# Performance work log

Hardware: AMD Instinct MI355X
Metric: run time of the kernel (lower is better)

Reference implementation:

```python
import jax, jax.numpy as jnp
import numpy as np

V = 32000   # vocab.size
E = 512     # embed_dim
H = 512     # hidden_dim
L = 2       # num_layers
W = 32      # window_size
S = 512     # seq_len
B = 8       # batch


def setup_inputs() -> dict:
    key = jax.random.key(0)
    ks = jax.random.split(key, 2 + 4 * L)
    bound = 1.0 / np.sqrt(H)
    inp = {
        "encoder_input": jax.random.randint(ks[0], (S, B), 0, V),
        "embed_table": jax.random.normal(ks[1], (V, E), jnp.float32),
    }
    for l in range(L):
        in_dim = E if l == 0 else H
        k = ks[2 + 4 * l: 6 + 4 * l]
        inp[f"w_ih_{l}"] = jax.random.uniform(k[0], (4 * H, in_dim), jnp.float32, -bound, bound)
        inp[f"w_hh_{l}"] = jax.random.uniform(k[1], (4 * H, H), jnp.float32, -bound, bound)
        inp[f"b_ih_{l}"] = jax.random.uniform(k[2], (4 * H,), jnp.float32, -bound, bound)
        inp[f"b_hh_{l}"] = jax.random.uniform(k[3], (4 * H,), jnp.float32, -bound, bound)
    return inp


def _lstm_layer(x, mask, w_ih, w_hh, b_ih, b_hh):
    # x: [T, N, D]; mask: [T, N, 1]. Masked steps keep (h, c), so every window
    # effectively starts from a zero state at its first valid position (same as
    # running a fresh LSTM on each window, torch gate order i,f,g,o).
    N = x.shape[1]
    Hd = w_hh.shape[1]
    bias = b_ih + b_hh

    def step(carry, inp_):
        h, c = carry
        xt, mt = inp_
        gates = xt @ w_ih.T + h @ w_hh.T + bias  # [N, 4H]
        i, f, g, o = jnp.split(gates, 4, axis=-1)
        i = jax.nn.sigmoid(i)
        f = jax.nn.sigmoid(f)
        g = jnp.tanh(g)
        o = jax.nn.sigmoid(o)
        c_new = f * c + i * g
        h_new = o * jnp.tanh(c_new)
        h = jnp.where(mt, h_new, h)
        c = jnp.where(mt, c_new, c)
        return (h, c), h

    z = jnp.zeros((N, Hd), x.dtype)
    (h, _), ys = jax.lax.scan(step, (z, z), (x, mask))
    return ys, h


def reference(encoder_input, embed_table,
              w_ih_0, w_hh_0, b_ih_0, b_hh_0,
              w_ih_1, w_hh_1, b_ih_1, b_hh_1):
    emb = embed_table[encoder_input]              # [S, B, E]
    T = W + 1
    # window position t for target index i is i - W + t (invalid when < 0)
    pos = jnp.arange(S)[None, :] - W + jnp.arange(T)[:, None]  # [T, S]
    valid = pos >= 0
    windows = emb[jnp.clip(pos, 0)]               # [T, S, B, E]
    x = windows.reshape(T, S * B, E)
    mask = jnp.broadcast_to(valid[:, :, None], (T, S, B)).reshape(T, S * B, 1)

    params = [(w_ih_0, w_hh_0, b_ih_0, b_hh_0), (w_ih_1, w_hh_1, b_ih_1, b_hh_1)]
    h = None
    for (wi, wh, bi, bh) in params:
        x, h = _lstm_layer(x, mask, wi, wh, bi, bh)
    # original takes encoder_output at the last window position == final hidden
    return h.reshape(S, B, H)
```

## Files before the change

kernel.cpp:

```cpp
#include <hip/hip_runtime.h>
#include <stdint.h>

#define NROWS 4096
#define HDIM  512
#define GDIM  2048
#define WWIN  32

typedef __attribute__((ext_vector_type(8))) short short8;
typedef __attribute__((ext_vector_type(4))) float f32x4;

__device__ __forceinline__ unsigned short f2bf(float x){
  union { float f; unsigned int u; } v; v.f = x;
  unsigned int u = v.u + 0x7fffu + ((v.u >> 16) & 1u);
  return (unsigned short)(u >> 16);
}
__device__ __forceinline__ float bf2f(unsigned short u){
  union { unsigned int u; float f; } v; v.u = ((unsigned int)u) << 16; return v.f;
}

__device__ __forceinline__ void gld16(const void* g, void* l){
  __builtin_amdgcn_global_load_lds(
      (const __attribute__((address_space(1))) unsigned int*)g,
      (__attribute__((address_space(3))) unsigned int*)l, 16, 0, 0);
}

__device__ __forceinline__ float sigm(float x){ return 1.f/(1.f + __expf(-x)); }
__device__ __forceinline__ float tanh_f(float x){ return 1.f - 2.f/(1.f + __expf(2.f*x)); }

__device__ __forceinline__ void band_sync(unsigned* ctr, unsigned target){
  __syncthreads();
  if (threadIdx.x == 0){
    __hip_atomic_fetch_add(ctr, 1u, __ATOMIC_RELAXED, __HIP_MEMORY_SCOPE_AGENT);
    while (__hip_atomic_load(ctr, __ATOMIC_RELAXED, __HIP_MEMORY_SCOPE_AGENT) < target)
      __builtin_amdgcn_s_sleep(2);
  }
  asm volatile("" ::: "memory");
  __syncthreads();
}

__device__ __forceinline__ void gemm_tile_db(
    const char* A0, const char* A1, const char* Bsrc,
    int ldbB, int nk, int r0, int c0,
    char* smem, int wr, int wc, int lane, f32x4 acc[4][4])
{
  const int tid = threadIdx.x;
  const int oo0 = tid * 16;
  const int srow = oo0 >> 7;
  const int scb  = oo0 & 127;
  const size_t aOff = (size_t)(r0 + srow) * 1024 + scb;
  const size_t bOff = (size_t)(c0 + srow) * (size_t)ldbB + scb;

  auto STAGE = [&](int kk, int buf){
    const char* Ap = (kk < 8) ? A0 : A1;
    const size_t kbA = (size_t)(kk & 7) * 128;
    const size_t kbB = (size_t)kk * 128;
    char* AsB = smem + buf * 16384;
    char* BsB = smem + 32768 + buf * 16384;
    #pragma unroll
    for (int i = 0; i < 4; ++i){
      const size_t rstep = (size_t)i * 32;
      gld16(Ap   + aOff + rstep * 1024          + kbA, AsB + i*4096 + oo0);
      gld16(Bsrc + bOff + rstep * (size_t)ldbB  + kbB, BsB + i*4096 + oo0);
    }
  };

  STAGE(0, 0);
  __syncthreads();

  const int lr = lane & 15;
  const int lk = (lane >> 4) * 8;

  for (int kk = 0; kk < nk; ++kk){
    const int cur = kk & 1;
    if (kk + 1 < nk) STAGE(kk + 1, cur ^ 1);

    const unsigned short* As = (const unsigned short*)(smem + cur*16384);
    const unsigned short* Bs = (const unsigned short*)(smem + 32768 + cur*16384);
    short8 a[2][4], b[2][4];
    #pragma unroll
    for (int h = 0; h < 2; ++h){
      const int k32 = h * 32;
      #pragma unroll
      for (int m = 0; m < 4; ++m)
        a[h][m] = *(const short8*)(As + (64*wr + 16*m + lr)*64 + k32 + lk);
      #pragma unroll
      for (int n = 0; n < 4; ++n)
        b[h][n] = *(const short8*)(Bs + (64*wc + 16*n + lr)*64 + k32 + lk);
    }
    __builtin_amdgcn_s_setprio(1);
    #pragma unroll
    for (int h = 0; h < 2; ++h)
      #pragma unroll
      for (int m = 0; m < 4; ++m)
        #pragma unroll
        for (int n = 0; n < 4; ++n)
          acc[m][n] = __builtin_amdgcn_mfma_f32_16x16x32_bf16(a[h][m], b[h][n], acc[m][n], 0, 0, 0);
    __builtin_amdgcn_s_setprio(0);

    __syncthreads();
  }
}

__global__ void __launch_bounds__(256) prep_weights(
    const float* wih0, const float* whh0, const float* bih0, const float* bhh0,
    const float* wih1, const float* whh1, const float* bih1, const float* bhh1,
    unsigned short* BrIh0, unsigned short* Br0, unsigned short* Br1,
    float* bias0r, float* br1)
{
  const int j = blockIdx.x;
  const int g = j & 3, hd = j >> 2;
  const int r = g*512 + hd;
  for (int k = threadIdx.x; k < 512; k += 256){
    BrIh0[(size_t)j*512 + k]      = f2bf(wih0[(size_t)r*512 + k]);
    Br0  [(size_t)j*512 + k]      = f2bf(whh0[(size_t)r*512 + k]);
    Br1  [(size_t)j*1024 + k]     = f2bf(wih1[(size_t)r*512 + k]);
    Br1  [(size_t)j*1024 + 512+k] = f2bf(whh1[(size_t)r*512 + k]);
  }
  if (threadIdx.x == 0){
    bias0r[j] = bih0[r] + bhh0[r];
    br1[j]    = bih1[r] + bhh1[r];
  }
}

__global__ void __launch_bounds__(256) gather_embed(const int* enc, const float* tbl,
                                                    unsigned short* E)
{
  const int n = blockIdx.x;
  const int idx = enc[n];
  const float* src = tbl + (size_t)idx * 512;
  unsigned short* dst = E + (size_t)n * 512;
  for (int e = threadIdx.x; e < 512; e += 256) dst[e] = f2bf(src[e]);
}

__global__ void __launch_bounds__(256) p0_gemm(const unsigned short* E,
                                               const unsigned short* BrIh0,
                                               const float* bias0r,
                                               unsigned short* P0)
{
  __shared__ __align__(16) char smem[65536];
  const int tid  = threadIdx.x;
  const int lane = tid & 63, wid = tid >> 6;
  const int wr = wid >> 1, wc = wid & 1;
  const int bid = blockIdx.x;
  const int r0 = (bid >> 4) * 128, c0 = (bid & 15) * 128;
  f32x4 acc[4][4] = {};
  gemm_tile_db((const char*)E, nullptr, (const char*)BrIh0, 1024, 8,
               r0, c0, smem, wr, wc, lane, acc);
  #pragma unroll
  for (int m = 0; m < 4; ++m){
    const int rowb = r0 + 64*wr + 16*m + ((lane >> 4) << 2);
    #pragma unroll
    for (int n = 0; n < 4; ++n){
      const int colb = c0 + 64*wc + 16*n + (lane & 15);
      const float bs = bias0r[colb];
      #pragma unroll
      for (int r = 0; r < 4; ++r)
        P0[(size_t)(rowb + r)*GDIM + colb] = f2bf(acc[m][n][r] + bs);
    }
  }
}

__global__ void __launch_bounds__(256, 2) persist_kernel(
    unsigned short* h0, unsigned short* h1,
    const unsigned short* Br0, const unsigned short* Br1,
    const unsigned short* P0, const float* br1, float* out, unsigned* bar)
{
  extern __shared__ __align__(16) char smem[];

  const int bid  = blockIdx.x;
  const int colg = bid & 7;
  const int bl   = bid >> 3;
  const bool L1  = (bl & 1);
  const int rb   = bl >> 1;
  const int r0   = rb * 128;
  const int c0v  = colg * 256;

  const int tid  = threadIdx.x;
  const int lane = tid & 63, wid = tid >> 6;
  const int wn = wid;
  const int lr = lane & 15, sl = lane >> 4;
  const int ph = (sl ^ ((lr >> 1) & 3)) << 4;

  const int sbyteB = ((tid & 3) ^ ((tid >> 3) & 3)) << 4;
  const int ar   = tid >> 1;
  const int as0  = (tid & 1) * 2;
  const int akey = (ar >> 1) & 3;

  const char* Bp  = (const char*)(L1 ? Br1 : Br0);
  const int  ldbB = L1 ? 2048 : 1024;
  const int  nkt  = L1 ? 32 : 16;

  unsigned* ctr = bar + rb * 32;

  float creg[4][4][2];
  #pragma unroll
  for (int p = 0; p < 4; ++p)
    #pragma unroll
    for (int q = 0; q < 4; ++q){ creg[p][q][0] = 0.f; creg[p][q][1] = 0.f; }

  for (int tau = 0; tau <= 33; ++tau){
    const bool active = L1 ? (tau >= 1) : (tau <= 32);
    if (active){
      const int t  = L1 ? (tau - 1) : tau;
      const int pr = (tau + 1) & 1, pw = tau & 1;
      const unsigned short* hA0 = h0 + (size_t)pr * (NROWS*HDIM);
      const unsigned short* hA1 = h1 + (size_t)pr * (NROWS*HDIM);

      auto issueB = [&](int kt2){
        char* d = smem + 16384 + (size_t)(kt2 & 1) * 16384 + tid * 16;
        const char* s = Bp + (size_t)(c0v + (tid >> 2)) * (size_t)ldbB
                           + kt2 * 64 + sbyteB;
        #pragma unroll
        for (int i = 0; i < 4; ++i)
          gld16(s + (size_t)(i * 64) * (size_t)ldbB, d + i * 4096);
      };
      auto issueA = [&](int kt2, unsigned long long a[4]){
        const unsigned short* hs; int kE;
        if (!L1 || kt2 < 16){ hs = hA0; kE = kt2 * 32; }
        else                { hs = hA1; kE = (kt2 - 16) * 32; }
        const unsigned long long* p =
            (const unsigned long long*)(hs + (size_t)(r0 + ar) * 512 + kE + as0 * 8);
        a[0] = __hip_atomic_load(p+0, __ATOMIC_RELAXED, __HIP_MEMORY_SCOPE_AGENT);
        a[1] = __hip_atomic_load(p+1, __ATOMIC_RELAXED, __HIP_MEMORY_SCOPE_AGENT);
        a[2] = __hip_atomic_load(p+2, __ATOMIC_RELAXED, __HIP_MEMORY_SCOPE_AGENT);
        a[3] = __hip_atomic_load(p+3, __ATOMIC_RELAXED, __HIP_MEMORY_SCOPE_AGENT);
      };
      auto writeA = [&](int kt2, const unsigned long long a[4]){
        char* base = smem + (size_t)(kt2 & 1) * 8192 + ar * 64;
        char* p0 = base + ((as0 ^ akey) << 4);
        char* p1 = base + (((as0 + 1) ^ akey) << 4);
        *(unsigned long long*)(p0)     = a[0];
        *(unsigned long long*)(p0 + 8) = a[1];
        *(unsigned long long*)(p1)     = a[2];
        *(unsigned long long*)(p1 + 8) = a[3];
      };

      f32x4 acc[8][4] = {};
      unsigned long long areg[4];

      issueA(0, areg);
      issueB(0);
      writeA(0, areg);
      issueA(1, areg);
      asm volatile("s_waitcnt vmcnt(4)" ::: "memory");
      asm volatile("s_waitcnt lgkmcnt(0)" ::: "memory");
      __builtin_amdgcn_s_barrier();

      for (int kt = 0; kt < nkt; ++kt){
        if (kt + 1 < nkt) issueB(kt + 1);
        const char* Ab = smem + (size_t)(kt & 1) * 8192;
        const char* Bb = smem + 16384 + (size_t)(kt & 1) * 16384;
        short8 a[8], b[4];
        #pragma unroll
        for (int n = 0; n < 4; ++n)
          b[n] = *(const short8*)(Bb + (wn*64 + n*16 + lr)*64 + ph);
        #pragma unroll
        for (int m = 0; m < 8; ++m)
          a[m] = *(const short8*)(Ab + (m*16 + lr)*64 + ph);

        __builtin_amdgcn_s_setprio(1);
        #pragma unroll
        for (int m = 0; m < 8; ++m)
          #pragma unroll
          for (int n = 0; n < 4; ++n)
            acc[m][n] = __builtin_amdgcn_mfma_f32_16x16x32_bf16(a[m], b[n], acc[m][n], 0, 0, 0);
        __builtin_amdgcn_s_setprio(0);

        if (kt + 1 < nkt){
          writeA(kt + 1, areg);
          if (kt + 2 < nkt){
            issueA(kt + 2, areg);
            asm volatile("s_waitcnt vmcnt(4)" ::: "memory");
          } else {
            asm volatile("s_waitcnt vmcnt(0)" ::: "memory");
          }
          asm volatile("s_waitcnt lgkmcnt(0)" ::: "memory");
          __builtin_amdgcn_s_barrier();
        }
      }

      float* GLDS = (float*)smem;
      const int GST = 68;
      unsigned short* hw = (L1 ? h1 : h0) + (size_t)pw * (NROWS*HDIM);
      const bool finalStep = (L1 && t == 32);
      const int cbase = c0v >> 2;

      #pragma unroll
      for (int pass = 0; pass < 4; ++pass){
        __syncthreads();
        if (wn == pass){
          #pragma unroll
          for (int m = 0; m < 8; ++m){
            const int rowb = m*16 + (sl << 2);
            #pragma unroll
            for (int n = 0; n < 4; ++n){
              const int colb = n*16 + lr;
              const f32x4 v = acc[m][n];
              #pragma unroll
              for (int r = 0; r < 4; ++r)
                GLDS[(rowb + r)*GST + colb] = v[r];
            }
          }
        }
        __syncthreads();
        #pragma unroll
        for (int it = 0; it < 4; ++it){
          const int pid = it*256 + tid;
          const int row = pid >> 3;
          const int pl  = (pid & 7) * 2;
          const int rowg = r0 + row;
          const int hd0  = cbase + pass*16 + pl;
          const float* gp = &GLDS[row*GST + 4*pl];
          const float4 g0 = *(const float4*)gp;
          const float4 g1 = *(const float4*)(gp + 4);
          float gi0 = g0.x, gf0 = g0.y, gg0 = g0.z, go0 = g0.w;
          float gi1 = g1.x, gf1 = g1.y, gg1 = g1.z, go1 = g1.w;
          const int s  = rowg >> 3;
          const int bb = rowg & 7;
          const int pos = s - WWIN + t;
          if (!L1){
            const int p0r = (pos < 0 ? 0 : pos)*8 + bb;
            const uint4 pv = *(const uint4*)&P0[(size_t)p0r*GDIM + 4*hd0];
            gi0 += bf2f((unsigned short)(pv.x & 0xffff));
            gf0 += bf2f((unsigned short)(pv.x >> 16));
            gg0 += bf2f((unsigned short)(pv.y & 0xffff));
            go0 += bf2f((unsigned short)(pv.y >> 16));
            gi1 += bf2f((unsigned short)(pv.z & 0xffff));
            gf1 += bf2f((unsigned short)(pv.z >> 16));
            gg1 += bf2f((unsigned short)(pv.w & 0xffff));
            go1 += bf2f((unsigned short)(pv.w >> 16));
          } else {
            const float4 b0 = *(const float4*)&br1[4*hd0];
            const float4 b1 = *(const float4*)&br1[4*hd0 + 4];
            gi0 += b0.x; gf0 += b0.y; gg0 += b0.z; go0 += b0.w;
            gi1 += b1.x; gf1 += b1.y; gg1 += b1.z; go1 += b1.w;
          }
          float cp0 = creg[pass][it][0];
          float cp1 = creg[pass][it][1];
          float i0 = sigm(gi0), f0 = sigm(gf0), gA = tanh_f(gg0), o0 = sigm(go0);
          float i1 = sigm(gi1), f1 = sigm(gf1), gB = tanh_f(gg1), o1 = sigm(go1);
          float cn0 = f0*cp0 + i0*gA;
          float cn1 = f1*cp1 + i1*gB;
          float hn0 = o0*tanh_f(cn0);
          float hn1 = o1*tanh_f(cn1);
          if (pos < 0){ cn0 = 0.f; hn0 = 0.f; cn1 = 0.f; hn1 = 0.f; }
          creg[pass][it][0] = cn0;
          creg[pass][it][1] = cn1;
          const size_t sidx0 = (size_t)rowg*HDIM + hd0;
          if (finalStep){
            *(float2*)&out[sidx0] = make_float2(hn0, hn1);
          } else {
            const unsigned hp = (unsigned)f2bf(hn0) | ((unsigned)f2bf(hn1) << 16);
            __hip_atomic_store((unsigned*)&hw[sidx0], hp, __ATOMIC_RELAXED,
                               __HIP_MEMORY_SCOPE_AGENT);
          }
        }
      }
    }
    if (tau != 33) band_sync(ctr, 16u * (unsigned)(tau + 1));
  }
}

__global__ void __launch_bounds__(512, 2) step_kernel(
    unsigned short* h0, unsigned short* h1, float* c0b, float* c1b,
    const unsigned short* Br0, const unsigned short* Br1,
    const unsigned short* P0, const float* br1, float* out, int tau, int bidOff)
{
  extern __shared__ __align__(16) char smem[];

  const int x = blockIdx.x & 7, kq = blockIdx.x >> 3;
  int wk;
  if (gridDim.x == 256) wk = ((kq & 1) << 7) + x * 16 + (kq >> 1);
  else                  wk = x * 16 + kq;
  wk += bidOff;

  const bool L1 = (wk >= 128);
  const int t  = L1 ? (tau - 1) : tau;
  const int pr = (tau + 1) & 1, pw = tau & 1;
  const int lb = L1 ? (wk - 128) : wk;
  const int r0  = (lb >> 3) * 256;
  const int c0v = (lb & 7) * 256;

  const int tid  = threadIdx.x;
  const int lane = tid & 63;
  const int wid  = tid >> 6;
  const int wm = wid >> 2, wn = wid & 3;
  const int lr = lane & 15, sl = lane >> 4;

  const unsigned short* hA0 = h0 + (size_t)pr * (NROWS*HDIM);
  const unsigned short* hA1 = h1 + (size_t)pr * (NROWS*HDIM);
  const char* Bp  = (const char*)(L1 ? Br1 : Br0);
  const int  ldbB = L1 ? 2048 : 1024;
  const int  nkt  = L1 ? 32 : 16;

  const int srow  = tid >> 2;
  const int sbyte = ((tid & 3) ^ ((tid >> 3) & 3)) << 4;
  const int ph    = (sl ^ ((lr >> 1) & 3)) << 4;
  const int laneA = (wm*128 + lr) * 64 + ph;
  const int laneB = (wn*64  + lr) * 64 + ph;

  auto STAGE_A = [&](int kt2, int c){
    const char* Ap; int kB;
    if (!L1 || kt2 < 16){ Ap = (const char*)hA0; kB = kt2 * 64; }
    else                { Ap = (const char*)hA1; kB = (kt2 - 16) * 64; }
    gld16(Ap + (size_t)(r0 + c*128 + srow) * 1024 + kB + sbyte,
          smem + (size_t)(kt2 & 3) * 32768 + c*8192 + tid*16);
  };
  auto STAGE_B = [&](int kt2, int c){
    gld16(Bp + (size_t)(c0v + c*128 + srow) * (size_t)ldbB + kt2*64 + sbyte,
          smem + (size_t)(kt2 & 3) * 32768 + 16384 + c*8192 + tid*16);
  };

  f32x4 acc[8][4] = {};

  STAGE_A(0,0); STAGE_A(0,1); STAGE_B(0,0); STAGE_B(0,1);
  STAGE_A(1,0); STAGE_A(1,1); STAGE_B(1,0); STAGE_B(1,1);
  asm volatile("s_waitcnt vmcnt(4)" ::: "memory");
  __builtin_amdgcn_s_barrier();

  for (int kt = 0; kt < nkt; ++kt){
    const char* bufp = smem + (size_t)(kt & 3) * 32768;
    const bool st = (kt + 2) < nkt;
    short8 a0[4], a1[4], b[4];

    #pragma unroll
    for (int m = 0; m < 4; ++m) a0[m] = *(const short8*)(bufp + laneA + m*1024);
    #pragma unroll
    for (int n = 0; n < 4; ++n) b[n]  = *(const short8*)(bufp + 16384 + laneB + n*1024);
    if (st){ STAGE_A(kt+2, 0); STAGE_A(kt+2, 1); }
    __builtin_amdgcn_s_barrier();
    asm volatile("s_waitcnt lgkmcnt(0)" ::: "memory");
    __builtin_amdgcn_sched_barrier(0);
    __builtin_amdgcn_s_setprio(1);
    #pragma unroll
    for (int m = 0; m < 4; ++m)
      #pragma unroll
      for (int n = 0; n < 4; ++n)
        acc[m][n] = __builtin_amdgcn_mfma_f32_16x16x32_bf16(a0[m], b[n], acc[m][n], 0, 0, 0);
    __builtin_amdgcn_s_setprio(0);
    __builtin_amdgcn_s_barrier();

    #pragma unroll
    for (int m = 0; m < 4; ++m) a1[m] = *(const short8*)(bufp + laneA + (4+m)*1024);
    if (st){
      STAGE_B(kt+2, 0); STAGE_B(kt+2, 1);
      asm volatile("s_waitcnt vmcnt(4)" ::: "memory");
    } else {
      asm volatile("s_waitcnt vmcnt(0)" ::: "memory");
    }
    __builtin_amdgcn_s_barrier();
    asm volatile("s_waitcnt lgkmcnt(0)" ::: "memory");
    __builtin_amdgcn_sched_barrier(0);
    __builtin_amdgcn_s_setprio(1);
    #pragma unroll
    for (int m = 0; m < 4; ++m)
      #pragma unroll
      for (int n = 0; n < 4; ++n)
        acc[4+m][n] = __builtin_amdgcn_mfma_f32_16x16x32_bf16(a1[m], b[n], acc[4+m][n], 0, 0, 0);
    __builtin_amdgcn_s_setprio(0);
    __builtin_amdgcn_s_barrier();
  }

  float* GLDS = (float*)smem;
  const int GST = 68;
  float* cbuf = L1 ? c1b : c0b;
  unsigned short* hw = (L1 ? h1 : h0) + (size_t)pw * (NROWS*HDIM);
  const bool finalStep = (L1 && t == 32);

  for (int pass = 0; pass < 4; ++pass){
    __syncthreads();
    if (wn == pass){
      #pragma unroll
      for (int m = 0; m < 8; ++m){
        const int rowb = wm*128 + m*16 + (sl << 2);
        #pragma unroll
        for (int n = 0; n < 4; ++n){
          const int colb = n*16 + lr;
          const f32x4 v = acc[m][n];
          #pragma unroll
          for (int r = 0; r < 4; ++r)
            GLDS[(rowb + r)*GST + colb] = v[r];
        }
      }
    }
    __syncthreads();
    #pragma unroll
    for (int it = 0; it < 8; ++it){
      const int cid = it*512 + tid;
      const int row = cid >> 4;
      const int l   = cid & 15;
      const int rowg = r0 + row;
      const int hd   = (c0v >> 2) + pass*16 + l;
      float4 gv = *(const float4*)&GLDS[row*GST + 4*l];
      float gi = gv.x, gf = gv.y, gg = gv.z, go = gv.w;
      const int s  = rowg >> 3;
      const int bb = rowg & 7;
      const int pos = s - WWIN + t;
      if (!L1){
        const int p0r = (pos < 0 ? 0 : pos)*8 + bb;
        const ushort4 pv = *(const ushort4*)&P0[(size_t)p0r*GDIM + 4*hd];
        gi += bf2f(pv.x); gf += bf2f(pv.y); gg += bf2f(pv.z); go += bf2f(pv.w);
      } else {
        float4 bv = *(const float4*)&br1[4*hd];
        gi += bv.x; gf += bv.y; gg += bv.z; go += bv.w;
      }
      const size_t sidx = (size_t)rowg*HDIM + hd;
      float cp = cbuf[sidx];
      float i_ = sigm(gi), f_ = sigm(gf), g_ = tanh_f(gg), o_ = sigm(go);
      float cn = f_*cp + i_*g_;
      float hn = o_*tanh_f(cn);
      if (pos < 0){ cn = 0.f; hn = 0.f; }
      cbuf[sidx] = cn;
      if (finalStep) out[sidx] = hn;
      else           hw[sidx]  = f2bf(hn);
    }
  }
}

extern "C" void kernel_launch(void* const* d_in, const int* in_sizes, int n_in,
                              void* d_out, int out_size, void* d_ws, size_t ws_size,
                              hipStream_t stream)
{
  const int*   enc  = (const int*)d_in[0];
  const float* tbl  = (const float*)d_in[1];
  const float* wih0 = (const float*)d_in[2];
  const float* whh0 = (const float*)d_in[3];
  const float* bih0 = (const float*)d_in[4];
  const float* bhh0 = (const float*)d_in[5];
  const float* wih1 = (const float*)d_in[6];
  const float* whh1 = (const float*)d_in[7];
  const float* bih1 = (const float*)d_in[8];
  const float* bhh1 = (const float*)d_in[9];
  float* out = (float*)d_out;

  char* ws = (char*)d_ws;
  size_t off = 0;
  auto alloc = [&](size_t bytes){
    char* p = ws + off; off += (bytes + 255) & ~(size_t)255; return p;
  };
  unsigned short* E     = (unsigned short*)alloc((size_t)NROWS*512*2);
  unsigned short* BrIh0 = (unsigned short*)alloc((size_t)GDIM*512*2);
  unsigned short* Br0   = (unsigned short*)alloc((size_t)GDIM*512*2);
  unsigned short* Br1   = (unsigned short*)alloc((size_t)GDIM*1024*2);
  float* bias0r = (float*)alloc(GDIM*4);
  float* br1    = (float*)alloc(GDIM*4);
  unsigned short* P0 = (unsigned short*)alloc((size_t)NROWS*GDIM*2);
  unsigned short* h0 = (unsigned short*)alloc((size_t)2*NROWS*HDIM*2);
  unsigned short* h1 = (unsigned short*)alloc((size_t)2*NROWS*HDIM*2);
  float* c0 = (float*)alloc((size_t)NROWS*HDIM*4);
  float* c1 = (float*)alloc((size_t)NROWS*HDIM*4);
  unsigned* bar = (unsigned*)alloc(4096);
  if (off > ws_size) return;

  (void)hipFuncSetAttribute(reinterpret_cast<const void*>(persist_kernel),
                            hipFuncAttributeMaxDynamicSharedMemorySize, 65536);
  (void)hipFuncSetAttribute(reinterpret_cast<const void*>(step_kernel),
                            hipFuncAttributeMaxDynamicSharedMemorySize, 131072);

  hipMemsetAsync(h0, 0, (size_t)33558528, stream);

  prep_weights<<<2048, 256, 0, stream>>>(wih0, whh0, bih0, bhh0,
                                         wih1, whh1, bih1, bhh1,
                                         BrIh0, Br0, Br1, bias0r, br1);
  gather_embed<<<4096, 256, 0, stream>>>(enc, tbl, E);
  p0_gemm<<<512, 256, 0, stream>>>(E, BrIh0, bias0r, P0);

  int occ = 0;
  hipError_t oe = hipOccupancyMaxActiveBlocksPerMultiprocessor(
      &occ, reinterpret_cast<const void*>(persist_kernel), 256, 49152);
  bool coop = (oe == hipSuccess && occ >= 2);
  if (coop){
    void* kargs[] = {&h0, &h1, &Br0, &Br1, &P0, &br1, &out, &bar};
    hipError_t le = hipLaunchCooperativeKernel(
        reinterpret_cast<const void*>(persist_kernel),
        dim3(512), dim3(256), kargs, 49152, stream);
    if (le != hipSuccess) coop = false;
  }
  if (!coop){
    for (int tau = 0; tau <= 33; ++tau){
      const int grid = (tau == 0 || tau == 33) ? 128 : 256;
      const int boff = (tau == 33) ? 128 : 0;
      step_kernel<<<grid, 512, 131072, stream>>>(h0, h1, c0, c1, Br0, Br1,
                                                 P0, br1, out, tau, boff);
    }
  }
}
```

Baseline: 1.738 ms.

## Retile persistent LSTM kernel to 64-row bands with 1024-column halves

```diff
diff --git a/kernel.cpp b/kernel.cpp
--- a/kernel.cpp
+++ b/kernel.cpp
@@ -160,7 +160,7 @@
   }
 }
 
-__global__ void __launch_bounds__(256, 2) persist_kernel(
+__global__ void __launch_bounds__(512, 1) persist_kernel(
     unsigned short* h0, unsigned short* h1,
     const unsigned short* Br0, const unsigned short* Br1,
     const unsigned short* P0, const float* br1, float* out, unsigned* bar)
@@ -168,29 +168,34 @@
   extern __shared__ __align__(16) char smem[];
 
   const int bid  = blockIdx.x;
-  const int colg = bid & 7;
-  const int bl   = bid >> 3;
-  const bool L1  = (bl & 1);
-  const int rb   = bl >> 1;
-  const int r0   = rb * 128;
-  const int c0v  = colg * 256;
+  const int x    = bid & 7;
+  const int s    = bid >> 3;
+  const bool L1  = (x & 1);
+  const int half = (x >> 1) & 1;
+  const int band = ((x >> 2) << 5) + s;
+  const int r0   = band * 64;
+  const int gbase  = half * 1024;
+  const int hdbase = half * 256;
 
   const int tid  = threadIdx.x;
-  const int lane = tid & 63, wid = tid >> 6;
-  const int wn = wid;
+  const int lane = tid & 63, wn = tid >> 6;
   const int lr = lane & 15, sl = lane >> 4;
-  const int ph = (sl ^ ((lr >> 1) & 3)) << 4;
-
-  const int sbyteB = ((tid & 3) ^ ((tid >> 3) & 3)) << 4;
-  const int ar   = tid >> 1;
-  const int as0  = (tid & 1) * 2;
-  const int akey = (ar >> 1) & 3;
+
+  const int sb8   = (tid & 7) ^ ((tid >> 3) & 7);
+  const int kslB  = sb8 & 3;
+  const int rhiB  = sb8 >> 2;
+  const int trlB  = (tid >> 3) << 1;
+  const int ar  = tid >> 3;
+  const int ac  = tid & 7;
+  const int alin  = ar >> 1;
+  const int asl8  = (((ar & 1) << 2) + (ac >> 1)) ^ (alin & 7);
+  const int awoff = alin*128 + asl8*16 + (ac & 1)*8;
 
   const char* Bp  = (const char*)(L1 ? Br1 : Br0);
-  const int  ldbB = L1 ? 2048 : 1024;
+  const int  ldb  = L1 ? 2048 : 1024;
   const int  nkt  = L1 ? 32 : 16;
 
-  unsigned* ctr = bar + rb * 32;
+  unsigned* ctr = bar + band * 32;
 
   float creg[4][4][2];
   #pragma unroll
@@ -207,94 +212,93 @@
       const unsigned short* hA1 = h1 + (size_t)pr * (NROWS*HDIM);
 
       auto issueB = [&](int kt2){
-        char* d = smem + 16384 + (size_t)(kt2 & 1) * 16384 + tid * 16;
-        const char* s = Bp + (size_t)(c0v + (tid >> 2)) * (size_t)ldbB
-                           + kt2 * 64 + sbyteB;
-        #pragma unroll
-        for (int i = 0; i < 4; ++i)
-          gld16(s + (size_t)(i * 64) * (size_t)ldbB, d + i * 4096);
+        char* d = smem + 16384 + (size_t)(kt2 & 1) * 65536 + tid * 16;
+        const int kb = kt2 * 64 + kslB * 16;
+        #pragma unroll
+        for (int i = 0; i < 8; ++i){
+          const int row = i*128 + trlB + rhiB;
+          gld16(Bp + (size_t)(gbase + row) * (size_t)ldb + kb, d + i*8192);
+        }
       };
-      auto issueA = [&](int kt2, unsigned long long a[4]){
+      auto issueA = [&](int kt2, unsigned long long& a){
         const unsigned short* hs; int kE;
         if (!L1 || kt2 < 16){ hs = hA0; kE = kt2 * 32; }
         else                { hs = hA1; kE = (kt2 - 16) * 32; }
         const unsigned long long* p =
-            (const unsigned long long*)(hs + (size_t)(r0 + ar) * 512 + kE + as0 * 8);
-        a[0] = __hip_atomic_load(p+0, __ATOMIC_RELAXED, __HIP_MEMORY_SCOPE_AGENT);
-        a[1] = __hip_atomic_load(p+1, __ATOMIC_RELAXED, __HIP_MEMORY_SCOPE_AGENT);
-        a[2] = __hip_atomic_load(p+2, __ATOMIC_RELAXED, __HIP_MEMORY_SCOPE_AGENT);
-        a[3] = __hip_atomic_load(p+3, __ATOMIC_RELAXED, __HIP_MEMORY_SCOPE_AGENT);
+            (const unsigned long long*)(hs + (size_t)(r0 + ar) * 512 + kE + ac * 4);
+        a = __hip_atomic_load(p, __ATOMIC_RELAXED, __HIP_MEMORY_SCOPE_AGENT);
       };
-      auto writeA = [&](int kt2, const unsigned long long a[4]){
-        char* base = smem + (size_t)(kt2 & 1) * 8192 + ar * 64;
-        char* p0 = base + ((as0 ^ akey) << 4);
-        char* p1 = base + (((as0 + 1) ^ akey) << 4);
-        *(unsigned long long*)(p0)     = a[0];
-        *(unsigned long long*)(p0 + 8) = a[1];
-        *(unsigned long long*)(p1)     = a[2];
-        *(unsigned long long*)(p1 + 8) = a[3];
+      auto writeA = [&](int kt2, unsigned long long a){
+        *(unsigned long long*)(smem + (size_t)(kt2 & 1) * 4096 + awoff) = a;
       };
 
-      f32x4 acc[8][4] = {};
-      unsigned long long areg[4];
+      f32x4 acc[4][8] = {};
+      unsigned long long areg;
 
       issueA(0, areg);
+      writeA(0, areg);
       issueB(0);
-      writeA(0, areg);
       issueA(1, areg);
-      asm volatile("s_waitcnt vmcnt(4)" ::: "memory");
+      asm volatile("s_waitcnt vmcnt(1)" ::: "memory");
       asm volatile("s_waitcnt lgkmcnt(0)" ::: "memory");
       __builtin_amdgcn_s_barrier();
 
       for (int kt = 0; kt < nkt; ++kt){
-        if (kt + 1 < nkt) issueB(kt + 1);
-        const char* Ab = smem + (size_t)(kt & 1) * 8192;
-        const char* Bb = smem + 16384 + (size_t)(kt & 1) * 16384;
-        short8 a[8], b[4];
-        #pragma unroll
-        for (int n = 0; n < 4; ++n)
-          b[n] = *(const short8*)(Bb + (wn*64 + n*16 + lr)*64 + ph);
-        #pragma unroll
-        for (int m = 0; m < 8; ++m)
-          a[m] = *(const short8*)(Ab + (m*16 + lr)*64 + ph);
+        if (kt + 1 < nkt){
+          writeA(kt + 1, areg);
+          issueB(kt + 1);
+          if (kt + 2 < nkt) issueA(kt + 2, areg);
+        }
+
+        const char* Ab = smem + (size_t)(kt & 1) * 4096;
+        const char* Bb = smem + 16384 + (size_t)(kt & 1) * 65536;
+        short8 a[4], b[8];
+        #pragma unroll
+        for (int m = 0; m < 4; ++m){
+          const int row = m*16 + lr;
+          const int ln  = row >> 1;
+          const int p8  = (((row & 1) << 2) + sl) ^ (ln & 7);
+          a[m] = *(const short8*)(Ab + ln*128 + p8*16);
+        }
+        #pragma unroll
+        for (int n = 0; n < 8; ++n){
+          const int row = wn*128 + n*16 + lr;
+          const int ln  = row >> 1;
+          const int p8  = (((row & 1) << 2) + sl) ^ (ln & 7);
+          b[n] = *(const short8*)(Bb + ln*128 + p8*16);
+        }
 
         __builtin_amdgcn_s_setprio(1);
         #pragma unroll
-        for (int m = 0; m < 8; ++m)
+        for (int m = 0; m < 4; ++m)
           #pragma unroll
-          for (int n = 0; n < 4; ++n)
+          for (int n = 0; n < 8; ++n)
             acc[m][n] = __builtin_amdgcn_mfma_f32_16x16x32_bf16(a[m], b[n], acc[m][n], 0, 0, 0);
         __builtin_amdgcn_s_setprio(0);
 
         if (kt + 1 < nkt){
-          writeA(kt + 1, areg);
-          if (kt + 2 < nkt){
-            issueA(kt + 2, areg);
-            asm volatile("s_waitcnt vmcnt(4)" ::: "memory");
-          } else {
-            asm volatile("s_waitcnt vmcnt(0)" ::: "memory");
-          }
+          if (kt + 2 < nkt) asm volatile("s_waitcnt vmcnt(1)" ::: "memory");
+          else              asm volatile("s_waitcnt vmcnt(0)" ::: "memory");
           asm volatile("s_waitcnt lgkmcnt(0)" ::: "memory");
           __builtin_amdgcn_s_barrier();
         }
       }
 
       float* GLDS = (float*)smem;
-      const int GST = 68;
+      const int GST = 260;
       unsigned short* hw = (L1 ? h1 : h0) + (size_t)pw * (NROWS*HDIM);
       const bool finalStep = (L1 && t == 32);
-      const int cbase = c0v >> 2;
 
       #pragma unroll
       for (int pass = 0; pass < 4; ++pass){
         __syncthreads();
-        if (wn == pass){
+        if ((wn >> 1) == pass){
           #pragma unroll
-          for (int m = 0; m < 8; ++m){
+          for (int m = 0; m < 4; ++m){
             const int rowb = m*16 + (sl << 2);
             #pragma unroll
-            for (int n = 0; n < 4; ++n){
-              const int colb = n*16 + lr;
+            for (int n = 0; n < 8; ++n){
+              const int colb = ((wn & 1) << 7) + n*16 + lr;
               const f32x4 v = acc[m][n];
               #pragma unroll
               for (int r = 0; r < 4; ++r)
@@ -305,19 +309,19 @@
         __syncthreads();
         #pragma unroll
         for (int it = 0; it < 4; ++it){
-          const int pid = it*256 + tid;
-          const int row = pid >> 3;
-          const int pl  = (pid & 7) * 2;
+          const int pid = it*512 + tid;
+          const int row = pid >> 5;
+          const int pl  = (pid & 31) * 2;
           const int rowg = r0 + row;
-          const int hd0  = cbase + pass*16 + pl;
+          const int hd0  = hdbase + pass*64 + pl;
           const float* gp = &GLDS[row*GST + 4*pl];
           const float4 g0 = *(const float4*)gp;
           const float4 g1 = *(const float4*)(gp + 4);
           float gi0 = g0.x, gf0 = g0.y, gg0 = g0.z, go0 = g0.w;
           float gi1 = g1.x, gf1 = g1.y, gg1 = g1.z, go1 = g1.w;
-          const int s  = rowg >> 3;
+          const int sI = rowg >> 3;
           const int bb = rowg & 7;
-          const int pos = s - WWIN + t;
+          const int pos = sI - WWIN + t;
           if (!L1){
             const int p0r = (pos < 0 ? 0 : pos)*8 + bb;
             const uint4 pv = *(const uint4*)&P0[(size_t)p0r*GDIM + 4*hd0];
@@ -357,7 +361,7 @@
         }
       }
     }
-    if (tau != 33) band_sync(ctr, 16u * (unsigned)(tau + 1));
+    if (tau != 33) band_sync(ctr, 4u * (unsigned)(tau + 1));
   }
 }
 
@@ -549,15 +553,15 @@
   unsigned short* h1 = (unsigned short*)alloc((size_t)2*NROWS*HDIM*2);
   float* c0 = (float*)alloc((size_t)NROWS*HDIM*4);
   float* c1 = (float*)alloc((size_t)NROWS*HDIM*4);
-  unsigned* bar = (unsigned*)alloc(4096);
+  unsigned* bar = (unsigned*)alloc(8192);
   if (off > ws_size) return;
 
   (void)hipFuncSetAttribute(reinterpret_cast<const void*>(persist_kernel),
-                            hipFuncAttributeMaxDynamicSharedMemorySize, 65536);
+                            hipFuncAttributeMaxDynamicSharedMemorySize, 147456);
   (void)hipFuncSetAttribute(reinterpret_cast<const void*>(step_kernel),
                             hipFuncAttributeMaxDynamicSharedMemorySize, 131072);
 
-  hipMemsetAsync(h0, 0, (size_t)33558528, stream);
+  hipMemsetAsync(h0, 0, (size_t)33562624, stream);
 
   prep_weights<<<2048, 256, 0, stream>>>(wih0, whh0, bih0, bhh0,
                                          wih1, whh1, bih1, bhh1,
@@ -567,13 +571,13 @@
 
   int occ = 0;
   hipError_t oe = hipOccupancyMaxActiveBlocksPerMultiprocessor(
-      &occ, reinterpret_cast<const void*>(persist_kernel), 256, 49152);
-  bool coop = (oe == hipSuccess && occ >= 2);
+      &occ, reinterpret_cast<const void*>(persist_kernel), 512, 147456);
+  bool coop = (oe == hipSuccess && occ >= 1);
   if (coop){
     void* kargs[] = {&h0, &h1, &Br0, &Br1, &P0, &br1, &out, &bar};
     hipError_t le = hipLaunchCooperativeKernel(
         reinterpret_cast<const void*>(persist_kernel),
-        dim3(512), dim3(256), kargs, 49152, stream);
+        dim3(256), dim3(512), kargs, 147456, stream);
     if (le != hipSuccess) coop = false;
   }
   if (!coop){
```

Measured after the change: 1.743 ms. No clear change (+0.3%).
